# Kernel tuning notes

Measured on AMD Instinct MI355X. Metric: run time of the kernel, lower is better.

## Reference

```python
import jax, jax.numpy as jnp
import numpy as np

D_MODEL = 1024
D_K = 1024
D_V = 1024
B = 4
S = 4096


def apply_rope(x, cos, sin):
    # x: [B, S, D]; cos/sin: [S, D//2] (broadcast over batch)
    d_half = x.shape[-1] // 2
    x0, x1 = x[..., :d_half], x[..., d_half:]
    return jnp.concatenate([x0 * cos - x1 * sin, x0 * sin + x1 * cos], axis=-1)


def setup_inputs() -> dict:
    key = jax.random.key(0)
    ks = jax.random.split(key, 9)
    x = jax.random.normal(ks[0], (B, S, D_MODEL), dtype=jnp.float32)
    cos = jax.random.uniform(ks[1], (S, D_K // 2), dtype=jnp.float32)
    sin = jax.random.uniform(ks[2], (S, D_K // 2), dtype=jnp.float32)
    # nn.Linear params: weight [out, in], bias [out]
    sq = 1.0 / np.sqrt(D_MODEL)
    W_q = jax.random.uniform(ks[3], (D_K, D_MODEL), minval=-sq, maxval=sq)
    b_q = jax.random.uniform(ks[4], (D_K,), minval=-sq, maxval=sq)
    W_k = jax.random.uniform(ks[5], (D_K, D_MODEL), minval=-sq, maxval=sq)
    b_k = jax.random.uniform(ks[6], (D_K,), minval=-sq, maxval=sq)
    W_v = jax.random.uniform(ks[7], (D_V, D_MODEL), minval=-sq, maxval=sq)
    b_v = jax.random.uniform(ks[8], (D_V,), minval=-sq, maxval=sq)
    return {"x": x, "cos": cos, "sin": sin, "W_q": W_q, "b_q": b_q,
            "W_k": W_k, "b_k": b_k, "W_v": W_v, "b_v": b_v}


def reference(x, cos, sin, W_q, b_q, W_k, b_k, W_v, b_v):
    seq_len = x.shape[1]
    Q = jnp.einsum('bsm,km->bsk', x, W_q) + b_q
    K = jnp.einsum('bsm,km->bsk', x, W_k) + b_k
    Q = apply_rope(Q, cos, sin)
    K = apply_rope(K, cos, sin)
    scores = jnp.einsum('bqk,btk->bqt', Q, K) / jnp.sqrt(jnp.float32(D_K))
    causal = jnp.tril(jnp.ones((seq_len, seq_len), dtype=bool))  # [S, S]
    scores = jnp.where(causal, scores, -jnp.inf)
    attn = jax.nn.softmax(scores, axis=-1)
    V = jnp.einsum('bsm,vm->bsv', x, W_v) + b_v
    z = jnp.einsum('bqt,btv->bqv', attn, V)
    return z
```

## Files before the change

### kernel.cpp

```cpp
#include <hip/hip_runtime.h>
#include <cstdint>
#include <cstddef>

using short8   = __attribute__((ext_vector_type(8))) short;
using f32x4    = __attribute__((ext_vector_type(4))) float;
using ushort4v = __attribute__((ext_vector_type(4))) unsigned short;

#define DEV static __device__ __forceinline__

constexpr int NB  = 4;
constexpr int SEQ = 4096;
constexpr int DM  = 1024;
constexpr int BSR = NB * SEQ;
constexpr size_t PBSTR = 136ULL * 65536;

DEV unsigned short f2bf(float f) {
  union { float f; unsigned u; } v; v.f = f;
  unsigned r = v.u + 0x7FFFu + ((v.u >> 16) & 1u);
  return (unsigned short)(r >> 16);
}

DEV int tri(int t) { return t * (t + 1) / 2; }

DEV void gload_lds16(const void* g, void* l) {
  __builtin_amdgcn_global_load_lds(
      (__attribute__((address_space(1))) void*)(g),
      (__attribute__((address_space(3))) void*)(l), 16, 0, 0);
}

DEV f32x4 mfma16(short8 a, short8 b, f32x4 c) {
  return __builtin_amdgcn_mfma_f32_16x16x32_bf16(a, b, c, 0, 0, 0);
}

DEV void bar() { asm volatile("s_barrier" ::: "memory"); }

DEV int orig_row(int p) {
  int gI = p >> 5, rr = p & 31;
  return (rr < 16) ? (gI * 16 + rr) : (512 + gI * 16 + (rr - 16));
}

__global__ __launch_bounds__(256) void convert_kernel(
    const float* __restrict__ x,
    const float* __restrict__ Wq, const float* __restrict__ Wk, const float* __restrict__ Wv,
    const float* __restrict__ bq, const float* __restrict__ bk, const float* __restrict__ bv,
    unsigned short* __restrict__ xbf,
    unsigned short* __restrict__ Wqp, unsigned short* __restrict__ Wkp, unsigned short* __restrict__ Wvp,
    float* __restrict__ bqp, float* __restrict__ bkp, float* __restrict__ bvp)
{
  const int U1 = BSR * DM / 8;
  const int U2 = 2 * DM * DM / 8;
  const int U3 = DM * DM / 8;
  const int U4 = 3 * DM / 8;
  const int total = U1 + U2 + U3 + U4;
  for (int u = blockIdx.x * blockDim.x + threadIdx.x; u < total;
       u += gridDim.x * blockDim.x) {
    if (u < U1) {
      int e = u * 8;
      float4 f0 = ((const float4*)(x + e))[0];
      float4 f1 = ((const float4*)(x + e))[1];
      short8 o;
      o[0]=(short)f2bf(f0.x); o[1]=(short)f2bf(f0.y); o[2]=(short)f2bf(f0.z); o[3]=(short)f2bf(f0.w);
      o[4]=(short)f2bf(f1.x); o[5]=(short)f2bf(f1.y); o[6]=(short)f2bf(f1.z); o[7]=(short)f2bf(f1.w);
      *(short8*)(xbf + e) = o;
    } else if (u < U1 + U2) {
      int w = u - U1;
      int which = w >> 17;
      int r = w & (131072 - 1);
      int p = r >> 7;
      int m8 = (r & 127) * 8;
      const float* src = (which ? Wk : Wq) + (size_t)orig_row(p) * DM + m8;
      unsigned short* dst = (which ? Wkp : Wqp) + (size_t)p * DM + m8;
      float4 f0 = ((const float4*)src)[0];
      float4 f1 = ((const float4*)src)[1];
      short8 o;
      o[0]=(short)f2bf(f0.x); o[1]=(short)f2bf(f0.y); o[2]=(short)f2bf(f0.z); o[3]=(short)f2bf(f0.w);
      o[4]=(short)f2bf(f1.x); o[5]=(short)f2bf(f1.y); o[6]=(short)f2bf(f1.z); o[7]=(short)f2bf(f1.w);
      *(short8*)dst = o;
    } else if (u < U1 + U2 + U3) {
      int r = u - (U1 + U2);
      int p = r >> 7;
      int m8 = (r & 127) * 8;
      const float* src = Wv + (size_t)p * DM + m8;
      float4 f0 = ((const float4*)src)[0];
      float4 f1 = ((const float4*)src)[1];
      short8 o;
      o[0]=(short)f2bf(f0.x); o[1]=(short)f2bf(f0.y); o[2]=(short)f2bf(f0.z); o[3]=(short)f2bf(f0.w);
      o[4]=(short)f2bf(f1.x); o[5]=(short)f2bf(f1.y); o[6]=(short)f2bf(f1.z); o[7]=(short)f2bf(f1.w);
      *(short8*)(Wvp + (size_t)p * DM + m8) = o;
    } else {
      int t = u - (U1 + U2 + U3);
      int which = t >> 7;
      int i0 = (t & 127) * 8;
      for (int e = 0; e < 8; ++e) {
        int p = i0 + e;
        if (which == 0)      bqp[p] = bq[orig_row(p)];
        else if (which == 1) bkp[p] = bk[orig_row(p)];
        else                 bvp[p] = bv[p];
      }
    }
  }
}


template <int DB, int MH, int KS, bool RB, int SREG, bool DOVM>
DEV void phase8(unsigned short* lds, const unsigned short* SG, int scol,
                const int (&aoff)[2][4], const int (&boff)[4], int tid,
                short8 (&bv)[4], f32x4 (&acc)[8][4])
{
  if (DOVM) asm volatile("s_waitcnt vmcnt(6)" ::: "memory");
  gload_lds16(SG + (size_t)(tid >> 2) * 1024 + scol,
              (void*)(lds + SREG + tid * 8));
  gload_lds16(SG + (size_t)((tid >> 2) + 128) * 1024 + scol,
              (void*)(lds + SREG + 4096 + tid * 8));
  short8 av[4];
  #pragma unroll
  for (int f = 0; f < 4; ++f)
    av[f] = *(const short8*)(lds + DB + KS * 8192 + aoff[MH][f]);
  if (RB) {
    #pragma unroll
    for (int f = 0; f < 4; ++f)
      bv[f] = *(const short8*)(lds + DB + 16384 + KS * 8192 + boff[f]);
  }
  bar();
  __builtin_amdgcn_s_setprio(1);
  #pragma unroll
  for (int fm = 0; fm < 4; ++fm)
    #pragma unroll
    for (int fn = 0; fn < 4; ++fn)
      acc[MH * 4 + fm][fn] = mfma16(av[fm], bv[fn], acc[MH * 4 + fm][fn]);
  __builtin_amdgcn_s_setprio(0);
  bar();
}

DEV void run_gemm8(unsigned short* lds,
                   const unsigned short* __restrict__ Ag,
                   const unsigned short* __restrict__ Bg,
                   int tid, int lane, int wm, int wn,
                   f32x4 (&acc)[8][4])
{
  const int c = lane & 15, g = lane >> 4;
  const int gsw = (g ^ ((c >> 1) & 3)) * 8;
  const int scg = (((tid & 3) ^ ((tid >> 3) & 3))) * 8;
  int aoff[2][4], boff[4];
  #pragma unroll
  for (int mh = 0; mh < 2; ++mh)
    #pragma unroll
    for (int f = 0; f < 4; ++f)
      aoff[mh][f] = (wm * 128 + mh * 64 + f * 16 + c) * 32 + gsw;
  #pragma unroll
  for (int f = 0; f < 4; ++f)
    boff[f] = (wn * 64 + f * 16 + c) * 32 + gsw;

  {
    const int r0 = tid >> 2;
    gload_lds16(Ag + (size_t)r0 * 1024 + scg,              (void*)(lds + tid * 8));
    gload_lds16(Ag + (size_t)(r0 + 128) * 1024 + scg,      (void*)(lds + 4096 + tid * 8));
    gload_lds16(Bg + (size_t)r0 * 1024 + scg,              (void*)(lds + 16384 + tid * 8));
    gload_lds16(Bg + (size_t)(r0 + 128) * 1024 + scg,      (void*)(lds + 16384 + 4096 + tid * 8));
    gload_lds16(Ag + (size_t)r0 * 1024 + 32 + scg,         (void*)(lds + 8192 + tid * 8));
    gload_lds16(Ag + (size_t)(r0 + 128) * 1024 + 32 + scg, (void*)(lds + 8192 + 4096 + tid * 8));
    gload_lds16(Bg + (size_t)r0 * 1024 + 32 + scg,         (void*)(lds + 24576 + tid * 8));
    gload_lds16(Bg + (size_t)(r0 + 128) * 1024 + 32 + scg, (void*)(lds + 24576 + 4096 + tid * 8));
    gload_lds16(Ag + (size_t)r0 * 1024 + 64 + scg,         (void*)(lds + 32768 + tid * 8));
    gload_lds16(Ag + (size_t)(r0 + 128) * 1024 + 64 + scg, (void*)(lds + 32768 + 4096 + tid * 8));
    gload_lds16(Bg + (size_t)r0 * 1024 + 64 + scg,         (void*)(lds + 49152 + tid * 8));
    gload_lds16(Bg + (size_t)(r0 + 128) * 1024 + 64 + scg, (void*)(lds + 49152 + 4096 + tid * 8));
  }
  asm volatile("s_waitcnt vmcnt(4)" ::: "memory");
  bar();

  short8 bv[4];
  for (int it = 0; it < 8; ++it) {
    const int s1 = 2 * it + 1;
    const int s2 = (2 * it + 2 < 16) ? 2 * it + 2 : 15;
    const int s3 = (2 * it + 3 < 16) ? 2 * it + 3 : 15;
    const int c1  = s1 * 64 + 32 + scg;
    const int c2a = s2 * 64 + scg;
    const int c2b = s2 * 64 + 32 + scg;
    const int c3  = s3 * 64 + scg;
    phase8<0,     0, 0, true,  40960, false>(lds, Ag, c1,  aoff, boff, tid, bv, acc);
    phase8<0,     1, 0, false, 57344, true >(lds, Bg, c1,  aoff, boff, tid, bv, acc);
    phase8<0,     0, 1, true,  0,     false>(lds, Ag, c2a, aoff, boff, tid, bv, acc);
    phase8<0,     1, 1, false, 16384, true >(lds, Bg, c2a, aoff, boff, tid, bv, acc);
    phase8<32768, 0, 0, true,  8192,  false>(lds, Ag, c2b, aoff, boff, tid, bv, acc);
    phase8<32768, 1, 0, false, 24576, true >(lds, Bg, c2b, aoff, boff, tid, bv, acc);
    phase8<32768, 0, 1, true,  32768, false>(lds, Ag, c3,  aoff, boff, tid, bv, acc);
    phase8<32768, 1, 1, false, 49152, true >(lds, Bg, c3,  aoff, boff, tid, bv, acc);
  }
  asm volatile("s_waitcnt vmcnt(0)" ::: "memory");
}

template <int MODE>
__global__ __launch_bounds__(512, 2) void k_gemm256(
    const unsigned short* __restrict__ Ain,
    const unsigned short* __restrict__ Bin,
    const float* __restrict__ bias,
    const float* __restrict__ cosT, const float* __restrict__ sinT,
    unsigned short* __restrict__ out, int b0, int G)
{
  __shared__ unsigned short lds[65536];
  const int tid = threadIdx.x, lane = tid & 63, wid = tid >> 6;
  const int wm = wid >> 2, wn = wid & 3;
  const int c = lane & 15, g = lane >> 4;

  if (MODE == 2) {
    const int xcd = blockIdx.x & 7, idx = blockIdx.x >> 3;
    const int njobs = (idx < G) ? 2 : 1;
    for (int jj = 0; jj < njobs; ++jj) {
      const int lin = xcd * (17 * G) + ((jj == 0) ? idx : 16 * G + idx);
      const int li = lin / 136;
      const int t136 = lin - li * 136;
      int tm = (int)((sqrtf(8.0f * (float)t136 + 1.0f) - 1.0f) * 0.5f);
      while (tri(tm + 1) <= t136) ++tm;
      while (tri(tm) > t136) --tm;
      const int tn = t136 - tri(tm);
      const int b = b0 + li;
      const int bm = tm * 256, bn = tn * 256;
      const unsigned short* Ag = Ain + ((size_t)b * SEQ + bm) * DM;
      const unsigned short* Bg = Bin + ((size_t)b * SEQ + bn) * DM;

      f32x4 z4 = {0.f, 0.f, 0.f, 0.f};
      f32x4 acc[8][4];
      #pragma unroll
      for (int m = 0; m < 8; ++m)
        #pragma unroll
        for (int n = 0; n < 4; ++n) acc[m][n] = z4;

      run_gemm8(lds, Ag, Bg, tid, lane, wm, wn, acc);

      const size_t Kp = (size_t)(tm + 1) * 256;
      unsigned short* pb = out + (size_t)li * PBSTR + (size_t)tri(tm) * 65536;
      #pragma unroll
      for (int am = 0; am < 8; ++am) {
        int lrow = wm * 128 + (am >> 2) * 64 + (am & 3) * 16 + g * 4;
        #pragma unroll
        for (int fn = 0; fn < 4; ++fn) {
          int col = bn + wn * 64 + fn * 16 + c;
          #pragma unroll
          for (int r = 0; r < 4; ++r) {
            union { _Float16 h; unsigned short u; } cv;
            cv.h = (_Float16)acc[am][fn][r];
            pb[(size_t)(lrow + r) * Kp + col] = cv.u;
          }
        }
      }
      __syncthreads();
    }
    return;
  }

  int xcd = blockIdx.x & 7, idx = blockIdx.x >> 3;
  const int bm = (xcd * 8 + (idx >> 2)) * 256;
  const int bn = (idx & 3) * 256;
  const unsigned short* Ag = Ain + (size_t)bm * DM;
  const unsigned short* Bg = Bin + (size_t)bn * DM;

  f32x4 z4 = {0.f, 0.f, 0.f, 0.f};
  f32x4 acc[8][4];
  #pragma unroll
  for (int m = 0; m < 8; ++m)
    #pragma unroll
    for (int n = 0; n < 4; ++n) acc[m][n] = z4;

  run_gemm8(lds, Ag, Bg, tid, lane, wm, wn, acc);

  if (MODE == 0) {
    #pragma unroll
    for (int am = 0; am < 8; ++am) {
      int row0 = bm + wm * 128 + (am >> 2) * 64 + (am & 3) * 16 + g * 4;
      #pragma unroll
      for (int fp = 0; fp < 4; fp += 2) {
        int f_g = (bn >> 4) + wn * 4 + fp;
        float b0f = bias[f_g * 16 + c];
        float b1f = bias[f_g * 16 + 16 + c];
        int j = (f_g >> 1) * 16 + c;
        #pragma unroll
        for (int r = 0; r < 4; ++r) {
          int rowg = row0 + r;
          int s = rowg & (SEQ - 1);
          float x0 = acc[am][fp][r] + b0f;
          float x1 = acc[am][fp + 1][r] + b1f;
          float cv = cosT[(size_t)s * (DM / 2) + j];
          float sv = sinT[(size_t)s * (DM / 2) + j];
          out[(size_t)rowg * DM + f_g * 16 + c]      = f2bf(x0 * cv - x1 * sv);
          out[(size_t)rowg * DM + f_g * 16 + 16 + c] = f2bf(x0 * sv + x1 * cv);
        }
      }
    }
  } else {
    #pragma unroll
    for (int am = 0; am < 8; ++am) {
      int s0 = bm + wm * 128 + (am >> 2) * 64 + (am & 3) * 16 + g * 4;
      int bb = s0 >> 12;
      int sl = s0 & (SEQ - 1);
      #pragma unroll
      for (int fn = 0; fn < 4; ++fn) {
        int v = bn + wn * 64 + fn * 16 + c;
        float bv_ = bias[v];
        ushort4v pk;
        #pragma unroll
        for (int r = 0; r < 4; ++r) pk[r] = f2bf(acc[am][fn][r] + bv_);
        *(ushort4v*)(out + ((size_t)(bb * DM + v)) * SEQ + sl) = pk;
      }
    }
  }
}

__global__ __launch_bounds__(256) void softmax_panel(unsigned short* __restrict__ S_)
{
  const int tid = threadIdx.x, wid = tid >> 6, lane = tid & 63;
  const int widx = blockIdx.x * 4 + wid;
  const int li = widx >> 12;
  const int r = widx & (SEQ - 1);
  const int p = r >> 8;
  const size_t Kp = (size_t)(p + 1) * 256;
  const int nt = p + 1;
  unsigned short* base = S_ + (size_t)li * PBSTR + (size_t)tri(p) * 65536 +
                         (size_t)(r & 255) * Kp;
  const float K2 = 0.04508422002778011f;

  float v[16][4];
  float mx = -3.0e38f;
  #pragma unroll
  for (int ch = 0; ch < 16; ++ch) {
    if (ch < nt) {
      uint2 u = *(const uint2*)(base + ch * 256 + lane * 4);
      union { unsigned u; _Float16 h[2]; } c0, c1;
      c0.u = u.x; c1.u = u.y;
      int col = ch * 256 + lane * 4;
      float a0 = (col     <= r) ? (float)c0.h[0] : -3.0e38f;
      float a1 = (col + 1 <= r) ? (float)c0.h[1] : -3.0e38f;
      float a2 = (col + 2 <= r) ? (float)c1.h[0] : -3.0e38f;
      float a3 = (col + 3 <= r) ? (float)c1.h[1] : -3.0e38f;
      v[ch][0] = a0; v[ch][1] = a1; v[ch][2] = a2; v[ch][3] = a3;
      mx = fmaxf(fmaxf(mx, fmaxf(a0, a1)), fmaxf(a2, a3));
    }
  }
  #pragma unroll
  for (int d = 1; d < 64; d <<= 1) mx = fmaxf(mx, __shfl_xor(mx, d, 64));
  float sum = 0.f;
  #pragma unroll
  for (int ch = 0; ch < 16; ++ch) {
    if (ch < nt) {
      #pragma unroll
      for (int e = 0; e < 4; ++e) {
        float pe = (v[ch][e] < -1.0e37f) ? 0.f : exp2f((v[ch][e] - mx) * K2);
        v[ch][e] = pe;
        sum += pe;
      }
    }
  }
  #pragma unroll
  for (int d = 1; d < 64; d <<= 1) sum += __shfl_xor(sum, d, 64);
  float inv = 1.0f / sum;
  #pragma unroll
  for (int ch = 0; ch < 16; ++ch) {
    if (ch < nt) {
      uint2 o;
      o.x = (unsigned)f2bf(v[ch][0] * inv) | ((unsigned)f2bf(v[ch][1] * inv) << 16);
      o.y = (unsigned)f2bf(v[ch][2] * inv) | ((unsigned)f2bf(v[ch][3] * inv) << 16);
      *(uint2*)(base + ch * 256 + lane * 4) = o;
    }
  }
}

template <int CN>
DEV void stage_pv(const unsigned short* g, size_t ld, size_t k0,
                  unsigned short* ldst, int sdst, int srow, int scg8) {
  #pragma unroll
  for (int cc = 0; cc < CN; ++cc)
    gload_lds16(g + (size_t)(cc * 128 + srow) * ld + k0 + scg8,
                (void*)(ldst + cc * 4096 + sdst));
}

DEV void run_gemm_pv(unsigned short* lds,
                     const unsigned short* __restrict__ Ag, size_t lda,
                     const unsigned short* __restrict__ Bg, size_t ldb,
                     int NT, int tid, int lane, int wm, int wn,
                     f32x4 (&acc)[4][4])
{
  constexpr int BUFE = (256 + 128) * 32;
  const int srow = tid >> 2;
  const int scg8 = (((tid & 3) ^ ((srow >> 1) & 3))) * 8;
  const int sdst = srow * 32 + (tid & 3) * 8;
  const int c = lane & 15, g = lane >> 4;
  const int gsw = (g ^ ((c >> 1) & 3)) * 8;
  int aoff[4], boff[4];
  #pragma unroll
  for (int f = 0; f < 4; ++f) aoff[f] = (wm * 64 + f * 16 + c) * 32 + gsw;
  #pragma unroll
  for (int f = 0; f < 4; ++f) boff[f] = 256 * 32 + (wn * 64 + f * 16 + c) * 32 + gsw;

  #pragma unroll
  for (int p = 0; p < 3; ++p) {
    stage_pv<2>(Ag, lda, (size_t)p * 32, lds + p * BUFE, sdst, srow, scg8);
    stage_pv<1>(Bg, ldb, (size_t)p * 32, lds + p * BUFE + 256 * 32, sdst, srow, scg8);
  }

  for (int t = 0; t < NT; ++t) {
    const int bsel = t & 3, nsel = (t + 3) & 3;
    const size_t ts = (size_t)((t + 3 < NT) ? t + 3 : NT - 1);
    unsigned short* lb = lds + bsel * BUFE;
    stage_pv<2>(Ag, lda, ts * 32, lds + nsel * BUFE, sdst, srow, scg8);
    asm volatile("s_waitcnt vmcnt(7)" ::: "memory");
    bar();
    short8 av[2], bv[4];
    #pragma unroll
    for (int f = 0; f < 2; ++f) av[f] = *(const short8*)(lb + aoff[f]);
    #pragma unroll
    for (int f = 0; f < 4; ++f) bv[f] = *(const short8*)(lb + boff[f]);
    __builtin_amdgcn_s_setprio(1);
    #pragma unroll
    for (int mf = 0; mf < 2; ++mf)
      #pragma unroll
      for (int nf = 0; nf < 4; ++nf)
        acc[mf][nf] = mfma16(av[mf], bv[nf], acc[mf][nf]);
    __builtin_amdgcn_s_setprio(0);
    stage_pv<1>(Bg, ldb, ts * 32, lds + nsel * BUFE + 256 * 32, sdst, srow, scg8);
    #pragma unroll
    for (int f = 0; f < 2; ++f) av[f] = *(const short8*)(lb + aoff[2 + f]);
    __builtin_amdgcn_s_setprio(1);
    #pragma unroll
    for (int mf = 0; mf < 2; ++mf)
      #pragma unroll
      for (int nf = 0; nf < 4; ++nf)
        acc[2 + mf][nf] = mfma16(av[mf], bv[nf], acc[2 + mf][nf]);
    __builtin_amdgcn_s_setprio(0);
    bar();
  }
  asm volatile("s_waitcnt vmcnt(0)" ::: "memory");
}

__global__ __launch_bounds__(512, 2) void k_pv(
    const unsigned short* __restrict__ P,
    const unsigned short* __restrict__ Vt,
    float* __restrict__ z, int b0, int G)
{
  __shared__ unsigned short lds[4 * 12288];
  const int tid = threadIdx.x, lane = tid & 63, wid = tid >> 6;
  const int wm = wid >> 1, wn = wid & 1;
  const int c = lane & 15, g = lane >> 4;
  const int x = blockIdx.x & 7;
  const int j = blockIdx.x >> 3;
  const int jid = x * G + (j >> 3);
  const int n8 = j & 7;
  const int li = jid >> 3;
  const int pl = jid & 7;
  const int b = b0 + li;
  const unsigned short* Bg = Vt + ((size_t)b * DM + n8 * 128) * SEQ;

  for (int h = 0; h < 2; ++h) {
    const int p = h ? (15 - pl) : pl;
    const int NT = (p + 1) * 8;
    const size_t Kp = (size_t)(p + 1) * 256;
    const unsigned short* panel = P + (size_t)li * PBSTR + (size_t)tri(p) * 65536;

    f32x4 z4 = {0.f, 0.f, 0.f, 0.f};
    f32x4 acc[4][4];
    #pragma unroll
    for (int m = 0; m < 4; ++m)
      #pragma unroll
      for (int n = 0; n < 4; ++n) acc[m][n] = z4;

    run_gemm_pv(lds, panel, Kp, Bg, SEQ, NT, tid, lane, wm, wn, acc);

    #pragma unroll
    for (int am = 0; am < 4; ++am) {
      int row = p * 256 + wm * 64 + am * 16 + g * 4;
      #pragma unroll
      for (int fn = 0; fn < 4; ++fn) {
        int col = n8 * 128 + wn * 64 + fn * 16 + c;
        #pragma unroll
        for (int r = 0; r < 4; ++r)
          z[((size_t)(b * SEQ + row + r)) * DM + col] = acc[am][fn][r];
      }
    }
    __syncthreads();
  }
}

extern "C" void kernel_launch(void* const* d_in, const int* in_sizes, int n_in,
                              void* d_out, int out_size, void* d_ws, size_t ws_size,
                              hipStream_t stream) {
  const float* x    = (const float*)d_in[0];
  const float* cosT = (const float*)d_in[1];
  const float* sinT = (const float*)d_in[2];
  const float* Wq   = (const float*)d_in[3];
  const float* bq   = (const float*)d_in[4];
  const float* Wk   = (const float*)d_in[5];
  const float* bk   = (const float*)d_in[6];
  const float* Wv   = (const float*)d_in[7];
  const float* bv   = (const float*)d_in[8];
  float* z = (float*)d_out;

  char* ws = (char*)d_ws;
  unsigned short* xbf = (unsigned short*)(ws);
  unsigned short* Wqp = (unsigned short*)(ws + 33554432);
  unsigned short* Wkp = (unsigned short*)(ws + 35651584);
  unsigned short* Wvp = (unsigned short*)(ws + 37748736);
  float* bqp = (float*)(ws + 39845888);
  float* bkp = (float*)(ws + 39849984);
  float* bvp = (float*)(ws + 39854080);
  unsigned short* Qbf = (unsigned short*)(ws + 39858176);
  unsigned short* Kbf = (unsigned short*)(ws + 73412608);
  unsigned short* Vtb = (unsigned short*)(ws + 106967040);
  const size_t BASE = 140521472ULL;
  const size_t PER  = PBSTR * 2ULL;
  unsigned short* Sc = (unsigned short*)(ws + BASE);

  int G = 1;
  if (ws_size >= BASE + 4 * PER)      G = 4;
  else if (ws_size >= BASE + 2 * PER) G = 2;

  convert_kernel<<<dim3(2048), dim3(256), 0, stream>>>(
      x, Wq, Wk, Wv, bq, bk, bv, xbf, Wqp, Wkp, Wvp, bqp, bkp, bvp);

  k_gemm256<0><<<dim3(256), dim3(512), 0, stream>>>(xbf, Wqp, bqp, cosT, sinT, Qbf, 0, 1);
  k_gemm256<0><<<dim3(256), dim3(512), 0, stream>>>(xbf, Wkp, bkp, cosT, sinT, Kbf, 0, 1);
  k_gemm256<1><<<dim3(256), dim3(512), 0, stream>>>(xbf, Wvp, bvp, cosT, sinT, Vtb, 0, 1);

  for (int b0 = 0; b0 < NB; b0 += G) {
    k_gemm256<2><<<dim3(128 * G), dim3(512), 0, stream>>>(Qbf, Kbf, nullptr, nullptr, nullptr, Sc, b0, G);
    softmax_panel<<<dim3(1024 * G), dim3(256), 0, stream>>>(Sc);
    k_pv<<<dim3(64 * G), dim3(512), 0, stream>>>(Sc, Vtb, z, b0, G);
  }
}
```

Baseline: 349.9 us.

## Skip upper-triangle MFMAs on diagonal score tiles and rebalance tile scheduling

For the G==4 case, the QK^T score kernel now assigns off-diagonal 256x256 tiles and diagonal tiles separately. Each block gets either two off-diagonal tiles or one off-diagonal tile plus two diagonal tiles. On diagonal tiles, a templated path skips MFMA fragments that lie entirely above the causal diagonal, so each diagonal tile costs roughly half the compute. The goal is to balance per-block work across 256 blocks and cut wasted matrix math on masked regions. The cost is more complex index decoding, and the causal-skip and rebalanced scheduling apply only when the workspace allows G==4.

```diff
diff --git a/kernel.cpp b/kernel.cpp
--- a/kernel.cpp
+++ b/kernel.cpp
@@ -102,10 +102,10 @@
 }
 
 
-template <int DB, int MH, int KS, bool RB, int SREG, bool DOVM>
+template <bool DIAG, int DB, int MH, int KS, bool RB, int SREG, bool DOVM>
 DEV void phase8(unsigned short* lds, const unsigned short* SG, int scol,
                 const int (&aoff)[2][4], const int (&boff)[4], int tid,
-                short8 (&bv)[4], f32x4 (&acc)[8][4])
+                int wm, int wn, short8 (&bv)[4], f32x4 (&acc)[8][4])
 {
   if (DOVM) asm volatile("s_waitcnt vmcnt(6)" ::: "memory");
   gload_lds16(SG + (size_t)(tid >> 2) * 1024 + scol,
@@ -126,12 +126,17 @@
   #pragma unroll
   for (int fm = 0; fm < 4; ++fm)
     #pragma unroll
-    for (int fn = 0; fn < 4; ++fn)
+    for (int fn = 0; fn < 4; ++fn) {
+      if (DIAG) {
+        if (wn * 4 + fn > wm * 8 + MH * 4 + fm) continue;
+      }
       acc[MH * 4 + fm][fn] = mfma16(av[fm], bv[fn], acc[MH * 4 + fm][fn]);
+    }
   __builtin_amdgcn_s_setprio(0);
   bar();
 }
 
+template <bool DIAG>
 DEV void run_gemm8(unsigned short* lds,
                    const unsigned short* __restrict__ Ag,
                    const unsigned short* __restrict__ Bg,
@@ -178,14 +183,14 @@
     const int c2a = s2 * 64 + scg;
     const int c2b = s2 * 64 + 32 + scg;
     const int c3  = s3 * 64 + scg;
-    phase8<0,     0, 0, true,  40960, false>(lds, Ag, c1,  aoff, boff, tid, bv, acc);
-    phase8<0,     1, 0, false, 57344, true >(lds, Bg, c1,  aoff, boff, tid, bv, acc);
-    phase8<0,     0, 1, true,  0,     false>(lds, Ag, c2a, aoff, boff, tid, bv, acc);
-    phase8<0,     1, 1, false, 16384, true >(lds, Bg, c2a, aoff, boff, tid, bv, acc);
-    phase8<32768, 0, 0, true,  8192,  false>(lds, Ag, c2b, aoff, boff, tid, bv, acc);
-    phase8<32768, 1, 0, false, 24576, true >(lds, Bg, c2b, aoff, boff, tid, bv, acc);
-    phase8<32768, 0, 1, true,  32768, false>(lds, Ag, c3,  aoff, boff, tid, bv, acc);
-    phase8<32768, 1, 1, false, 49152, true >(lds, Bg, c3,  aoff, boff, tid, bv, acc);
+    phase8<DIAG, 0,     0, 0, true,  40960, false>(lds, Ag, c1,  aoff, boff, tid, wm, wn, bv, acc);
+    phase8<DIAG, 0,     1, 0, false, 57344, true >(lds, Bg, c1,  aoff, boff, tid, wm, wn, bv, acc);
+    phase8<DIAG, 0,     0, 1, true,  0,     false>(lds, Ag, c2a, aoff, boff, tid, wm, wn, bv, acc);
+    phase8<DIAG, 0,     1, 1, false, 16384, true >(lds, Bg, c2a, aoff, boff, tid, wm, wn, bv, acc);
+    phase8<DIAG, 32768, 0, 0, true,  8192,  false>(lds, Ag, c2b, aoff, boff, tid, wm, wn, bv, acc);
+    phase8<DIAG, 32768, 1, 0, false, 24576, true >(lds, Bg, c2b, aoff, boff, tid, wm, wn, bv, acc);
+    phase8<DIAG, 32768, 0, 1, true,  32768, false>(lds, Ag, c3,  aoff, boff, tid, wm, wn, bv, acc);
+    phase8<DIAG, 32768, 1, 1, false, 49152, true >(lds, Bg, c3,  aoff, boff, tid, wm, wn, bv, acc);
   }
   asm volatile("s_waitcnt vmcnt(0)" ::: "memory");
 }
@@ -205,19 +210,51 @@
 
   if (MODE == 2) {
     const int xcd = blockIdx.x & 7, idx = blockIdx.x >> 3;
-    const int njobs = (idx < G) ? 2 : 1;
-    for (int jj = 0; jj < njobs; ++jj) {
-      const int lin = xcd * (17 * G) + ((jj == 0) ? idx : 16 * G + idx);
-      const int li = lin / 136;
-      const int t136 = lin - li * 136;
-      int tm = (int)((sqrtf(8.0f * (float)t136 + 1.0f) - 1.0f) * 0.5f);
-      while (tri(tm + 1) <= t136) ++tm;
-      while (tri(tm) > t136) --tm;
-      const int tn = t136 - tri(tm);
+    int nj;
+    int jli[3], jtm[3], jtn[3];
+    if (G == 4) {
+      int ods[3] = {-1, -1, -1}, dds[3] = {-1, -1, -1};
+      if (idx < 28) {
+        nj = 2;
+        ods[0] = 60 * xcd + 2 * idx;
+        ods[1] = 60 * xcd + 2 * idx + 1;
+      } else {
+        nj = 3;
+        int k = idx - 28;
+        ods[0] = 60 * xcd + 56 + k;
+        dds[1] = 8 * xcd + 2 * k;
+        dds[2] = 8 * xcd + 2 * k + 1;
+      }
+      for (int j = 0; j < nj; ++j) {
+        if (ods[j] >= 0) {
+          int li = ods[j] / 120;
+          int t = ods[j] - 120 * li;
+          int tm = (int)((1.0f + sqrtf(1.0f + 8.0f * (float)t)) * 0.5f);
+          while (tm * (tm - 1) / 2 > t) --tm;
+          while ((tm + 1) * tm / 2 <= t) ++tm;
+          jli[j] = li; jtm[j] = tm; jtn[j] = t - tm * (tm - 1) / 2;
+        } else {
+          jli[j] = dds[j] >> 4; jtm[j] = dds[j] & 15; jtn[j] = dds[j] & 15;
+        }
+      }
+    } else {
+      nj = (idx < G) ? 2 : 1;
+      for (int j = 0; j < nj; ++j) {
+        const int lin = xcd * (17 * G) + ((j == 0) ? idx : 16 * G + idx);
+        int li = lin / 136;
+        int t136 = lin - li * 136;
+        int tm = (int)((sqrtf(8.0f * (float)t136 + 1.0f) - 1.0f) * 0.5f);
+        while (tri(tm + 1) <= t136) ++tm;
+        while (tri(tm) > t136) --tm;
+        jli[j] = li; jtm[j] = tm; jtn[j] = t136 - tri(tm);
+      }
+    }
+
+    for (int j = 0; j < nj; ++j) {
+      const int li = jli[j], tm = jtm[j], tn = jtn[j];
       const int b = b0 + li;
-      const int bm = tm * 256, bn = tn * 256;
-      const unsigned short* Ag = Ain + ((size_t)b * SEQ + bm) * DM;
-      const unsigned short* Bg = Bin + ((size_t)b * SEQ + bn) * DM;
+      const unsigned short* Ag = Ain + ((size_t)b * SEQ + tm * 256) * DM;
+      const unsigned short* Bg = Bin + ((size_t)b * SEQ + tn * 256) * DM;
 
       f32x4 z4 = {0.f, 0.f, 0.f, 0.f};
       f32x4 acc[8][4];
@@ -226,7 +263,10 @@
         #pragma unroll
         for (int n = 0; n < 4; ++n) acc[m][n] = z4;
 
-      run_gemm8(lds, Ag, Bg, tid, lane, wm, wn, acc);
+      if (G == 4 && tm == tn)
+        run_gemm8<true>(lds, Ag, Bg, tid, lane, wm, wn, acc);
+      else
+        run_gemm8<false>(lds, Ag, Bg, tid, lane, wm, wn, acc);
 
       const size_t Kp = (size_t)(tm + 1) * 256;
       unsigned short* pb = out + (size_t)li * PBSTR + (size_t)tri(tm) * 65536;
@@ -235,7 +275,7 @@
         int lrow = wm * 128 + (am >> 2) * 64 + (am & 3) * 16 + g * 4;
         #pragma unroll
         for (int fn = 0; fn < 4; ++fn) {
-          int col = bn + wn * 64 + fn * 16 + c;
+          int col = tn * 256 + wn * 64 + fn * 16 + c;
           #pragma unroll
           for (int r = 0; r < 4; ++r) {
             union { _Float16 h; unsigned short u; } cv;
@@ -262,7 +302,7 @@
     #pragma unroll
     for (int n = 0; n < 4; ++n) acc[m][n] = z4;
 
-  run_gemm8(lds, Ag, Bg, tid, lane, wm, wn, acc);
+  run_gemm8<false>(lds, Ag, Bg, tid, lane, wm, wn, acc);
 
   if (MODE == 0) {
     #pragma unroll
@@ -520,7 +560,8 @@
   k_gemm256<1><<<dim3(256), dim3(512), 0, stream>>>(xbf, Wvp, bvp, cosT, sinT, Vtb, 0, 1);
 
   for (int b0 = 0; b0 < NB; b0 += G) {
-    k_gemm256<2><<<dim3(128 * G), dim3(512), 0, stream>>>(Qbf, Kbf, nullptr, nullptr, nullptr, Sc, b0, G);
+    const int nblk = (G == 4) ? 256 : 128 * G;
+    k_gemm256<2><<<dim3(nblk), dim3(512), 0, stream>>>(Qbf, Kbf, nullptr, nullptr, nullptr, Sc, b0, G);
     softmax_panel<<<dim3(1024 * G), dim3(256), 0, stream>>>(Sc);
     k_pv<<<dim3(64 * G), dim3(512), 0, stream>>>(Sc, Vtb, z, b0, G);
   }
```

After: 368.1 us. 1.05x slower.

## Rebalance causal QK^T tile scheduling with half-width tail tiles for G=4

Applied to the files above, without the earlier changes.

For the G=4 path, the QK^T scores kernel now assigns work per XCD so that each block handles two full 256x256 tiles. The leftover tiles are split into two 256x128 halves, computed with the existing PV GEMM routine and spread across the remaining blocks. This replaces the previous scheme in which a few blocks ran two tiles and the rest ran one, which left a long tail of imbalance. The grid is fixed at 256 blocks for G=4. The half-tile path uses a different MFMA tiling and adds code complexity.

```diff
diff --git a/kernel.cpp b/kernel.cpp
--- a/kernel.cpp
+++ b/kernel.cpp
@@ -190,6 +190,73 @@
   asm volatile("s_waitcnt vmcnt(0)" ::: "memory");
 }
 
+template <int CN>
+DEV void stage_pv(const unsigned short* g, size_t ld, size_t k0,
+                  unsigned short* ldst, int sdst, int srow, int scg8) {
+  #pragma unroll
+  for (int cc = 0; cc < CN; ++cc)
+    gload_lds16(g + (size_t)(cc * 128 + srow) * ld + k0 + scg8,
+                (void*)(ldst + cc * 4096 + sdst));
+}
+
+DEV void run_gemm_pv(unsigned short* lds,
+                     const unsigned short* __restrict__ Ag, size_t lda,
+                     const unsigned short* __restrict__ Bg, size_t ldb,
+                     int NT, int tid, int lane, int wm, int wn,
+                     f32x4 (&acc)[4][4])
+{
+  constexpr int BUFE = (256 + 128) * 32;
+  const int srow = tid >> 2;
+  const int scg8 = (((tid & 3) ^ ((srow >> 1) & 3))) * 8;
+  const int sdst = srow * 32 + (tid & 3) * 8;
+  const int c = lane & 15, g = lane >> 4;
+  const int gsw = (g ^ ((c >> 1) & 3)) * 8;
+  int aoff[4], boff[4];
+  #pragma unroll
+  for (int f = 0; f < 4; ++f) aoff[f] = (wm * 64 + f * 16 + c) * 32 + gsw;
+  #pragma unroll
+  for (int f = 0; f < 4; ++f) boff[f] = 256 * 32 + (wn * 64 + f * 16 + c) * 32 + gsw;
+
+  #pragma unroll
+  for (int p = 0; p < 3; ++p) {
+    stage_pv<2>(Ag, lda, (size_t)p * 32, lds + p * BUFE, sdst, srow, scg8);
+    stage_pv<1>(Bg, ldb, (size_t)p * 32, lds + p * BUFE + 256 * 32, sdst, srow, scg8);
+  }
+
+  for (int t = 0; t < NT; ++t) {
+    const int bsel = t & 3, nsel = (t + 3) & 3;
+    const size_t ts = (size_t)((t + 3 < NT) ? t + 3 : NT - 1);
+    unsigned short* lb = lds + bsel * BUFE;
+    stage_pv<2>(Ag, lda, ts * 32, lds + nsel * BUFE, sdst, srow, scg8);
+    asm volatile("s_waitcnt vmcnt(7)" ::: "memory");
+    bar();
+    short8 av[2], bv[4];
+    #pragma unroll
+    for (int f = 0; f < 2; ++f) av[f] = *(const short8*)(lb + aoff[f]);
+    #pragma unroll
+    for (int f = 0; f < 4; ++f) bv[f] = *(const short8*)(lb + boff[f]);
+    __builtin_amdgcn_s_setprio(1);
+    #pragma unroll
+    for (int mf = 0; mf < 2; ++mf)
+      #pragma unroll
+      for (int nf = 0; nf < 4; ++nf)
+        acc[mf][nf] = mfma16(av[mf], bv[nf], acc[mf][nf]);
+    __builtin_amdgcn_s_setprio(0);
+    stage_pv<1>(Bg, ldb, ts * 32, lds + nsel * BUFE + 256 * 32, sdst, srow, scg8);
+    #pragma unroll
+    for (int f = 0; f < 2; ++f) av[f] = *(const short8*)(lb + aoff[2 + f]);
+    __builtin_amdgcn_s_setprio(1);
+    #pragma unroll
+    for (int mf = 0; mf < 2; ++mf)
+      #pragma unroll
+      for (int nf = 0; nf < 4; ++nf)
+        acc[2 + mf][nf] = mfma16(av[mf], bv[nf], acc[2 + mf][nf]);
+    __builtin_amdgcn_s_setprio(0);
+    bar();
+  }
+  asm volatile("s_waitcnt vmcnt(0)" ::: "memory");
+}
+
 template <int MODE>
 __global__ __launch_bounds__(512, 2) void k_gemm256(
     const unsigned short* __restrict__ Ain,
@@ -205,19 +272,33 @@
 
   if (MODE == 2) {
     const int xcd = blockIdx.x & 7, idx = blockIdx.x >> 3;
-    const int njobs = (idx < G) ? 2 : 1;
-    for (int jj = 0; jj < njobs; ++jj) {
-      const int lin = xcd * (17 * G) + ((jj == 0) ? idx : 16 * G + idx);
-      const int li = lin / 136;
-      const int t136 = lin - li * 136;
+    int t0, t1, ths = -1, hh = 0;
+    if (G == 4) {
+      const int base = xcd * 68;
+      if (idx < 24) { t0 = base + 2 * idx; t1 = t0 + 1; }
+      else {
+        int k = idx - 24;
+        t0 = base + 48 + 2 * k; t1 = t0 + 1;
+        ths = base + 64 + (k >> 1); hh = k & 1;
+      }
+    } else {
+      const int lin0 = xcd * (17 * G) + idx;
+      t0 = lin0;
+      t1 = (idx < G) ? (xcd * (17 * G) + 16 * G + idx) : -1;
+    }
+
+    for (int j = 0; j < 2; ++j) {
+      const int t = j ? t1 : t0;
+      if (t < 0) break;
+      const int li = t / 136;
+      const int t136 = t - li * 136;
       int tm = (int)((sqrtf(8.0f * (float)t136 + 1.0f) - 1.0f) * 0.5f);
       while (tri(tm + 1) <= t136) ++tm;
       while (tri(tm) > t136) --tm;
       const int tn = t136 - tri(tm);
       const int b = b0 + li;
-      const int bm = tm * 256, bn = tn * 256;
-      const unsigned short* Ag = Ain + ((size_t)b * SEQ + bm) * DM;
-      const unsigned short* Bg = Bin + ((size_t)b * SEQ + bn) * DM;
+      const unsigned short* Ag = Ain + ((size_t)b * SEQ + tm * 256) * DM;
+      const unsigned short* Bg = Bin + ((size_t)b * SEQ + tn * 256) * DM;
 
       f32x4 z4 = {0.f, 0.f, 0.f, 0.f};
       f32x4 acc[8][4];
@@ -235,7 +316,7 @@
         int lrow = wm * 128 + (am >> 2) * 64 + (am & 3) * 16 + g * 4;
         #pragma unroll
         for (int fn = 0; fn < 4; ++fn) {
-          int col = bn + wn * 64 + fn * 16 + c;
+          int col = tn * 256 + wn * 64 + fn * 16 + c;
           #pragma unroll
           for (int r = 0; r < 4; ++r) {
             union { _Float16 h; unsigned short u; } cv;
@@ -245,6 +326,45 @@
         }
       }
       __syncthreads();
+    }
+
+    if (ths >= 0) {
+      const int wmp = wid >> 1, wnp = wid & 1;
+      const int li = ths / 136;
+      const int t136 = ths - li * 136;
+      int tm = (int)((sqrtf(8.0f * (float)t136 + 1.0f) - 1.0f) * 0.5f);
+      while (tri(tm + 1) <= t136) ++tm;
+      while (tri(tm) > t136) --tm;
+      const int tn = t136 - tri(tm);
+      const int b = b0 + li;
+      const unsigned short* Ag = Ain + ((size_t)b * SEQ + tm * 256) * DM;
+      const unsigned short* Bg = Bin + ((size_t)b * SEQ + tn * 256 + hh * 128) * DM;
+
+      f32x4 z4 = {0.f, 0.f, 0.f, 0.f};
+      f32x4 acch[4][4];
+      #pragma unroll
+      for (int m = 0; m < 4; ++m)
+        #pragma unroll
+        for (int n = 0; n < 4; ++n) acch[m][n] = z4;
+
+      run_gemm_pv(lds, Ag, DM, Bg, DM, 32, tid, lane, wmp, wnp, acch);
+
+      const size_t Kp = (size_t)(tm + 1) * 256;
+      unsigned short* pb = out + (size_t)li * PBSTR + (size_t)tri(tm) * 65536;
+      #pragma unroll
+      for (int am = 0; am < 4; ++am) {
+        int lrow = wmp * 64 + am * 16 + g * 4;
+        #pragma unroll
+        for (int fn = 0; fn < 4; ++fn) {
+          int col = tn * 256 + hh * 128 + wnp * 64 + fn * 16 + c;
+          #pragma unroll
+          for (int r = 0; r < 4; ++r) {
+            union { _Float16 h; unsigned short u; } cv;
+            cv.h = (_Float16)acch[am][fn][r];
+            pb[(size_t)(lrow + r) * Kp + col] = cv.u;
+          }
+        }
+      }
     }
     return;
   }
@@ -362,73 +482,6 @@
       *(uint2*)(base + ch * 256 + lane * 4) = o;
     }
   }
-}
-
-template <int CN>
-DEV void stage_pv(const unsigned short* g, size_t ld, size_t k0,
-                  unsigned short* ldst, int sdst, int srow, int scg8) {
-  #pragma unroll
-  for (int cc = 0; cc < CN; ++cc)
-    gload_lds16(g + (size_t)(cc * 128 + srow) * ld + k0 + scg8,
-                (void*)(ldst + cc * 4096 + sdst));
-}
-
-DEV void run_gemm_pv(unsigned short* lds,
-                     const unsigned short* __restrict__ Ag, size_t lda,
-                     const unsigned short* __restrict__ Bg, size_t ldb,
-                     int NT, int tid, int lane, int wm, int wn,
-                     f32x4 (&acc)[4][4])
-{
-  constexpr int BUFE = (256 + 128) * 32;
-  const int srow = tid >> 2;
-  const int scg8 = (((tid & 3) ^ ((srow >> 1) & 3))) * 8;
-  const int sdst = srow * 32 + (tid & 3) * 8;
-  const int c = lane & 15, g = lane >> 4;
-  const int gsw = (g ^ ((c >> 1) & 3)) * 8;
-  int aoff[4], boff[4];
-  #pragma unroll
-  for (int f = 0; f < 4; ++f) aoff[f] = (wm * 64 + f * 16 + c) * 32 + gsw;
-  #pragma unroll
-  for (int f = 0; f < 4; ++f) boff[f] = 256 * 32 + (wn * 64 + f * 16 + c) * 32 + gsw;
-
-  #pragma unroll
-  for (int p = 0; p < 3; ++p) {
-    stage_pv<2>(Ag, lda, (size_t)p * 32, lds + p * BUFE, sdst, srow, scg8);
-    stage_pv<1>(Bg, ldb, (size_t)p * 32, lds + p * BUFE + 256 * 32, sdst, srow, scg8);
-  }
-
-  for (int t = 0; t < NT; ++t) {
-    const int bsel = t & 3, nsel = (t + 3) & 3;
-    const size_t ts = (size_t)((t + 3 < NT) ? t + 3 : NT - 1);
-    unsigned short* lb = lds + bsel * BUFE;
-    stage_pv<2>(Ag, lda, ts * 32, lds + nsel * BUFE, sdst, srow, scg8);
-    asm volatile("s_waitcnt vmcnt(7)" ::: "memory");
-    bar();
-    short8 av[2], bv[4];
-    #pragma unroll
-    for (int f = 0; f < 2; ++f) av[f] = *(const short8*)(lb + aoff[f]);
-    #pragma unroll
-    for (int f = 0; f < 4; ++f) bv[f] = *(const short8*)(lb + boff[f]);
-    __builtin_amdgcn_s_setprio(1);
-    #pragma unroll
-    for (int mf = 0; mf < 2; ++mf)
-      #pragma unroll
-      for (int nf = 0; nf < 4; ++nf)
-        acc[mf][nf] = mfma16(av[mf], bv[nf], acc[mf][nf]);
-    __builtin_amdgcn_s_setprio(0);
-    stage_pv<1>(Bg, ldb, ts * 32, lds + nsel * BUFE + 256 * 32, sdst, srow, scg8);
-    #pragma unroll
-    for (int f = 0; f < 2; ++f) av[f] = *(const short8*)(lb + aoff[2 + f]);
-    __builtin_amdgcn_s_setprio(1);
-    #pragma unroll
-    for (int mf = 0; mf < 2; ++mf)
-      #pragma unroll
-      for (int nf = 0; nf < 4; ++nf)
-        acc[2 + mf][nf] = mfma16(av[mf], bv[nf], acc[2 + mf][nf]);
-    __builtin_amdgcn_s_setprio(0);
-    bar();
-  }
-  asm volatile("s_waitcnt vmcnt(0)" ::: "memory");
 }
 
 __global__ __launch_bounds__(512, 2) void k_pv(
@@ -520,7 +573,8 @@
   k_gemm256<1><<<dim3(256), dim3(512), 0, stream>>>(xbf, Wvp, bvp, cosT, sinT, Vtb, 0, 1);
 
   for (int b0 = 0; b0 < NB; b0 += G) {
-    k_gemm256<2><<<dim3(128 * G), dim3(512), 0, stream>>>(Qbf, Kbf, nullptr, nullptr, nullptr, Sc, b0, G);
+    const int nblk = (G == 4) ? 256 : 128 * G;
+    k_gemm256<2><<<dim3(nblk), dim3(512), 0, stream>>>(Qbf, Kbf, nullptr, nullptr, nullptr, Sc, b0, G);
     softmax_panel<<<dim3(1024 * G), dim3(256), 0, stream>>>(Sc);
     k_pv<<<dim3(64 * G), dim3(512), 0, stream>>>(Sc, Vtb, z, b0, G);
   }
```

Result: slower. 357.8 us (+2.3%).
